# Kernel optimization log

Measured on AMD Instinct MI355X. Metric: run time of the kernel, lower is better.

The kernel has to match this reference:

```python
import jax, jax.numpy as jnp
import numpy as np

N, H, B, D, O = 512, 40, 8, 384, 62
DT = 1e-4  # step_size
BOUND = 500.0  # coupling saturation bound
# Jansen-Rit constants (ParamsJR defaults, all variances 0 -> non-learnable)
A_, a_, B_, b_, g_ = 3.25, 100.0, 22.0, 50.0, 100.0
c1, c2, c3, c4 = 135.0, 135.0 * 0.8, 135.0 * 0.25, 135.0 * 0.25
STD_IN, VMAX, V0, R_, MU, K_, KI = 100.0, 5.0, 6.0, 0.56, 0.5, 5.0, 1.0


def setup_inputs() -> dict:
    key = jax.random.key(0)
    ks = jax.random.split(key, 9)
    return {
        "input": jax.random.normal(ks[0], (N, H, B), jnp.float32),
        "noise_in": jax.random.normal(ks[1], (N, H, B, 1), jnp.float32),
        "noise_out": jax.random.normal(ks[2], (N, B), jnp.float32),
        "hx": jax.random.uniform(ks[3], (N, 6), jnp.float32),
        "hE": jax.random.normal(ks[4], (N, D), jnp.float32),
        "w_bb": jax.random.normal(ks[5], (N, N), jnp.float32),
        "sc": jax.random.uniform(ks[6], (N, N), jnp.float32),
        "lm": jax.random.normal(ks[7], (O, N), jnp.float32),
        "delays": jax.random.randint(ks[8], (N, N), 0, D, jnp.int32),
    }


def _sigmoid(x):
    # potential-to-rate operator
    return VMAX / (1.0 + jnp.exp(R_ * (V0 - x)))


def _sys2nd(Aamp, a, u, x, v):
    return Aamp * a * u - 2.0 * a * v - a * a * x


def reference(input, noise_in, noise_out, hx, hE, w_bb, sc, lm, delays):
    # normalized symmetric coupling matrix
    w = jnp.exp(w_bb) * sc
    ws = jnp.log1p(0.5 * (w + w.T))
    w_n = ws / jnp.linalg.norm(ws)            # Frobenius norm, as torch.linalg.norm
    rowsum = jnp.sum(w_n, axis=1)[:, None]    # dg = -diag(rowsum); dg @ x == -rowsum*x

    M, E, I = hx[:, 0:1], hx[:, 1:2], hx[:, 2:3]
    Mv, Ev, Iv = hx[:, 3:4], hx[:, 4:5], hx[:, 5:6]

    def hidden_step(carry, inp):
        M, E, I, Mv, Ev, Iv, hE = carry
        u, nz = inp  # [N,1] each
        Ed = jnp.take_along_axis(hE, delays, axis=1)      # Ed[i,j] = hE[i, delays[i,j]]
        LEd = jnp.sum(w_n * Ed.T, axis=1, keepdims=True)  # [N,1]
        noiseE = nz * STD_IN
        stim = K_ * KI * u
        rM = _sigmoid(E - I)
        rE = c2 * _sigmoid(c1 * M)
        rI = c4 * _sigmoid(c3 * M)
        coupled = g_ * (LEd - rowsum * (E - I))
        coupling = BOUND * jnp.tanh(coupled / BOUND)
        Mn = M + DT * Mv
        En = E + DT * Ev
        In = I + DT * Iv
        Mvn = Mv + DT * _sys2nd(A_, a_, rM, M, Mv)
        Evn = Ev + DT * _sys2nd(A_, a_, rE + coupling + stim + noiseE + MU, E, Ev)
        Ivn = Iv + DT * _sys2nd(B_, b_, rI, I, Iv)
        hE = hE.at[:, 0].set(En[:, 0] - In[:, 0])  # in-place slot-0 write, as in torch
        return (Mn, En, In, Mvn, Evn, Ivn, hE), None

    def batch_step(state, inp):
        u_seq, nz_seq = inp  # [H,N,1]
        state, _ = jax.lax.scan(hidden_step, state, (u_seq, nz_seq))
        M, E, I, Mv, Ev, Iv, hE = state
        hE = jnp.concatenate([E - I, hE[:, :-1]], axis=1)  # shift delay buffer
        eeg = 0.0005 * (lm @ (E - I))  # [O,1]
        return (M, E, I, Mv, Ev, Iv, hE), (M, E, I, Mv, Ev, Iv, eeg)

    u_all = jnp.transpose(input, (2, 1, 0))[..., None]            # [B,H,N,1]
    nz_all = jnp.transpose(noise_in[..., 0], (2, 1, 0))[..., None]
    state0 = (M, E, I, Mv, Ev, Iv, hE)
    state, outs = jax.lax.scan(batch_step, state0, (u_all, nz_all))
    Ms, Es, Is, Mvs, Evs, Ivs, eegs = outs  # [B,N,1] each, eeg [B,O,1]

    stack = lambda x: x[..., 0].T  # -> [N,B] (or [O,B]), matches torch.cat(axis=1)
    Mf, Ef, If, Mvf, Evf, Ivf, hEf = state
    current_state = jnp.concatenate([Mf, Ef, If, Mvf, Evf, Ivf], axis=1)  # [N,6]
    return (current_state, stack(eegs), stack(Es), stack(Is), stack(Ms),
            stack(Evs), stack(Ivs), stack(Mvs), hEf)
```

## Files before the change

kernel.cpp:

```cpp
#include <hip/hip_runtime.h>
#include <math.h>

#define N_    512
#define H_    40
#define B_N   8
#define D_    384
#define O_    62
#define RW    392
#define SMAX  13
#define CMAX  28
#define DRVS  336

#define OUT_STATE 0
#define OUT_EEG   3072
#define OUT_ES    3568
#define OUT_IS    7664
#define OUT_MS    11760
#define OUT_EVS   15856
#define OUT_IVS   19952
#define OUT_MVS   24048
#define OUT_HE    28144

#define SIGK      0.8079092228978195f
#define SIGC      4.847455337386917f
#define SIGK_E    109.06774509120563f
#define SIGK_I    27.266936272801407f
#define TANHS     0.5770780163555854f
#define C3Q       4.190944e-05f

#define BARRIER() asm volatile("s_waitcnt lgkmcnt(0)\n\ts_barrier" ::: "memory")

__global__ void k_cnt(const int* __restrict__ delays, int* __restrict__ s0c) {
    int i = blockIdx.x, t = threadIdx.x;
    bool f1 = (delays[t * N_ + i] == 0);
    bool f2 = (delays[(t + 256) * N_ + i] == 0);
    unsigned long long m1 = __ballot(f1), m2 = __ballot(f2);
    __shared__ int pc[4];
    int wave = t >> 6, lane = t & 63;
    if (lane == 0) pc[wave] = __popcll(m1) + __popcll(m2);
    __syncthreads();
    if (t == 0) {
        int s = pc[0] + pc[1] + pc[2] + pc[3];
        s0c[i] = (s > SMAX) ? SMAX : s;
    }
}

__global__ void __launch_bounds__(512)
k_perm(const int* __restrict__ s0c, int* __restrict__ perm,
       int* __restrict__ invp, int* __restrict__ wmaxc) {
    int t = threadIdx.x;
    int wave = t >> 6, lane = t & 63;
    int cnt = s0c[t];
    __shared__ int wc[14 * 8];
    __shared__ int base[14 * 8];
    unsigned long long below = (lane == 0) ? 0ull : ((~0ull) >> (64 - lane));
    for (int c = 0; c < 14; c++) {
        unsigned long long m = __ballot(cnt == c);
        if (lane == 0) wc[c * 8 + wave] = __popcll(m);
    }
    __syncthreads();
    if (t == 0) {
        int s = 0;
        for (int c = 0; c < 14; c++)
            for (int w = 0; w < 8; w++) { base[c * 8 + w] = s; s += wc[c * 8 + w]; }
    }
    __syncthreads();
    int pos = 0;
    for (int c = 0; c < 14; c++) {
        unsigned long long m = __ballot(cnt == c);
        if (cnt == c) pos = base[c * 8 + wave] + __popcll(m & below);
    }
    perm[pos] = t;
    invp[t] = pos;
    if ((pos & 63) == 63) wmaxc[pos >> 6] = cnt;
}

__global__ void k_prep(const float* __restrict__ wbb, const float* __restrict__ sc,
                       const float* __restrict__ hE_in, const int* __restrict__ delays,
                       const int* __restrict__ invp,
                       float* __restrict__ ws, float* __restrict__ ring,
                       float* __restrict__ rowsumP, float* __restrict__ sumsq,
                       float* __restrict__ s0w, int* __restrict__ s0j,
                       float* __restrict__ s1w, int* __restrict__ s1p) {
    int i = blockIdx.x;
    int t = threadIdx.x;
    int ip = invp[i];
    __shared__ float wsrow[N_];
    __shared__ float red[256];
    __shared__ int cnt_c[8];
    __shared__ int bases[8];
    __shared__ int runbase;

    if (t < SMAX) { s0j[t * N_ + ip] = i;        s0w[t * N_ + ip] = 0.f; }
    if (t < CMAX) { s1p[t * N_ + ip] = (1 << 9); s1w[t * N_ + ip] = 0.f; }
    if (t < 9)    { ring[i * RW + t] = 0.f; }

    float ssq = 0.f, rsum = 0.f;
    for (int j = t; j < N_; j += 256) {
        float w = 0.5f * (__expf(wbb[i * N_ + j]) * sc[i * N_ + j] +
                          __expf(wbb[j * N_ + i]) * sc[j * N_ + i]);
        float v = 0.6931471805599453f * __builtin_amdgcn_logf(1.0f + w);
        ws[i * N_ + j] = v;
        wsrow[j] = v;
        ssq += v * v;
        rsum += v;
    }
    for (int k = t; k < D_ - 1; k += 256) ring[i * RW + 9 + k] = hE_in[i * D_ + 1 + k];

    red[t] = ssq; __syncthreads();
    for (int s = 128; s > 0; s >>= 1) { if (t < s) red[t] += red[t + s]; __syncthreads(); }
    if (t == 0) sumsq[i] = red[0];
    __syncthreads();
    red[t] = rsum; __syncthreads();
    for (int s = 128; s > 0; s >>= 1) { if (t < s) red[t] += red[t + s]; __syncthreads(); }
    if (t == 0) rowsumP[ip] = red[0];
    __syncthreads();

    int wave = t >> 6, lane = t & 63;
    int dv1 = delays[t * N_ + i];
    int dv2 = delays[(t + 256) * N_ + i];
    unsigned long long below = (lane == 0) ? 0ull : ((~0ull) >> (64 - lane));
    for (int d = 0; d < 8; d++) {
        bool f1 = (dv1 == d), f2 = (dv2 == d);
        unsigned long long m1 = __ballot(f1);
        unsigned long long m2 = __ballot(f2);
        if (lane == 0) { cnt_c[wave] = __popcll(m1); cnt_c[wave + 4] = __popcll(m2); }
        __syncthreads();
        if (t == 0) {
            int s = (d == 0) ? 0 : runbase;
            for (int c = 0; c < 8; c++) { bases[c] = s; s += cnt_c[c]; }
            if (d == 0) runbase = 0;
            else runbase = s;
        }
        __syncthreads();
        if (d == 0) {
            if (f1) { int pos = bases[wave]     + __popcll(m1 & below);
                      if (pos < SMAX) { s0j[pos * N_ + ip] = t;       s0w[pos * N_ + ip] = wsrow[t]; } }
            if (f2) { int pos = bases[wave + 4] + __popcll(m2 & below);
                      if (pos < SMAX) { s0j[pos * N_ + ip] = t + 256; s0w[pos * N_ + ip] = wsrow[t + 256]; } }
        } else {
            if (f1) { int pos = bases[wave]     + __popcll(m1 & below);
                      if (pos < CMAX) { s1p[pos * N_ + ip] = t | (d << 9);         s1w[pos * N_ + ip] = wsrow[t]; } }
            if (f2) { int pos = bases[wave + 4] + __popcll(m2 & below);
                      if (pos < CMAX) { s1p[pos * N_ + ip] = (t + 256) | (d << 9); s1w[pos * N_ + ip] = wsrow[t + 256]; } }
        }
    }
}

__global__ void __launch_bounds__(512)
k_hist(const float* __restrict__ ws, const int* __restrict__ delays,
       const float* __restrict__ ring, const int* __restrict__ invp,
       const float* __restrict__ input, const float* __restrict__ noise_in,
       float* __restrict__ drv, float* __restrict__ bp8) {
    if (blockIdx.x < H_ * B_N) {
        int bb = blockIdx.x & 7, h = blockIdx.x >> 3;
        int step = bb * H_ + h;
        int nn = threadIdx.x;
        float u  = input[nn * (H_ * B_N) + h * B_N + bb];
        float nz = noise_in[nn * (H_ * B_N) + h * B_N + bb];
        drv[(size_t)invp[nn] * DRVS + step] = fmaf(0.1625f, u, fmaf(3.25f, nz, 16.26625f));
    }
    int b  = blockIdx.x >> 6;
    int ib = (blockIdx.x >> 3) & 7;
    int jb = blockIdx.x & 7;
    int wave = threadIdx.x >> 6, lane = threadIdx.x & 63;
    int i = ib * 64 + lane;
    int off = 8 - b;
    float acc = 0.f;
    int j0 = jb * 64 + wave * 8;
#pragma unroll
    for (int jj = 0; jj < 8; jj++) {
        int j = j0 + jj;
        int d = delays[j * N_ + i];
        float w = ws[j * N_ + i];
        float v = ring[j * RW + off + d];
        acc += (d > 0 ? w : 0.f) * v;
    }
    __shared__ float part[8][64];
    part[wave][lane] = acc; __syncthreads();
    if (wave == 0) {
        float s = 0.f;
#pragma unroll
        for (int w2 = 0; w2 < 8; w2++) s += part[w2][lane];
        bp8[(b * 8 + jb) * N_ + invp[i]] = s;
    }
}

#define LOADK0(K) int jb_##K = s0j[K * N_ + t] << 2; float w_##K = s0w[K * N_ + t] * scale;
#define GS(SLOT, K) (*(const float*)((const char*)curr4 + ((SLOT) << 11) + jb_##K))

#define PRFS(S, SLOT)                                                          \
    if (wmax > 0) { g##S##0 = GS(SLOT,0); g##S##1 = GS(SLOT,1); }              \
    if (wmax > 2) { g##S##2 = GS(SLOT,2); g##S##3 = GS(SLOT,3); }              \
    if (wmax > 4) { g##S##4 = GS(SLOT,4); g##S##5 = GS(SLOT,5);                \
                    g##S##6 = GS(SLOT,6); g##S##7 = GS(SLOT,7);                \
                    g##S##8 = GS(SLOT,8); g##S##9 = GS(SLOT,9);                \
                    g##S##10 = GS(SLOT,10); g##S##11 = GS(SLOT,11);            \
                    g##S##12 = GS(SLOT,12); }

#define STEPCORE(DV, S, WSLOT)                                                 \
  {                                                                            \
    float e0 = __builtin_amdgcn_exp2f(fmaf(-SIGK, ei_c, SIGC));                \
    float uu = __builtin_amdgcn_exp2f(fmaf(-SIGK_I, M, SIGC));                 \
    float u2 = uu * uu;                                                        \
    float u4 = u2 * u2;                                                        \
    float rMr = __builtin_amdgcn_rcpf(1.0f + e0);                              \
    float rIr = __builtin_amdgcn_rcpf(1.0f + uu);                              \
    float rEr = __builtin_amdgcn_rcpf(fmaf(C3Q, u4, 1.0f));                    \
    float En = fmaf(1e-4f, Ev, E);                                             \
    float In = fmaf(1e-4f, Iv, I);                                             \
    float Mn = fmaf(1e-4f, Mv, M);                                             \
    float a0 = 0.f, a1 = 0.f;                                                  \
    if (wmax > 0) { a0 = w_0 * g##S##0; a1 = w_1 * g##S##1; }                  \
    if (wmax > 2) { a0 = fmaf(w_2, g##S##2, a0); a1 = fmaf(w_3, g##S##3, a1); }\
    if (wmax > 4) { a0 = fmaf(w_4,  g##S##4,  a0); a1 = fmaf(w_5,  g##S##5,  a1);\
                    a0 = fmaf(w_6,  g##S##6,  a0); a1 = fmaf(w_7,  g##S##7,  a1);\
                    a0 = fmaf(w_8,  g##S##8,  a0); a1 = fmaf(w_9,  g##S##9,  a1);\
                    a0 = fmaf(w_10, g##S##10, a0); a1 = fmaf(w_11, g##S##11, a1);\
                    a0 = fmaf(w_12, g##S##12, a0); }                           \
    float arg = fmaf(-rs, ei_c, base) + (a0 + a1);                             \
    float e1 = __builtin_amdgcn_exp2f(arg);                                    \
    float cr = __builtin_amdgcn_rcpf(1.0f + e1);                               \
    float Mvn = fmaf(0.1625f,  rMr, fmaf(0.98f, Mv, -M));                      \
    float Ivn = fmaf(18.5625f, rIr, fmaf(0.99f, Iv, -0.25f * I));              \
    float Evn = fmaf(-32.5f, cr, fmaf(17.55f, rEr, fmaf(0.98f, Ev, -E) + (DV)));\
    float En2 = fmaf(1e-4f, Evn, En);                                          \
    float In2 = fmaf(1e-4f, Ivn, In);                                          \
    curr4[WSLOT][n] = En2 - In2;                                               \
    M = Mn; E = En; I = In; Mv = Mvn; Ev = Evn; Iv = Ivn;                      \
    ei_c = En - In;                                                            \
  }

#define BLOCK(S0, S1, W0, W1, DVA, DVB)                                        \
    PRFS(A, S0)                                                                \
    PRFS(B, S1)                                                                \
    STEPCORE(DVA, A, W0)                                                       \
    STEPCORE(DVB, B, W1)                                                       \
    BARRIER();

__global__ void __launch_bounds__(512)
k_hidden(const float* __restrict__ drv, const float* __restrict__ hE_in,
         const float* __restrict__ hx, const float* __restrict__ bp8,
         const float* __restrict__ sumsq, const float* __restrict__ rowsumP,
         const float* __restrict__ s0w, const int* __restrict__ s0j,
         const float* __restrict__ s1w, const int* __restrict__ s1p,
         const int* __restrict__ perm, const int* __restrict__ wmaxc,
         float* __restrict__ ring, float* __restrict__ fing,
         float* __restrict__ out) {
    __shared__ float curr4[4][N_];
    __shared__ float fin_l[B_N * N_];
    __shared__ float red[N_];
    int t = threadIdx.x;
    int n = perm[t];
    int wmax = __builtin_amdgcn_readfirstlane(wmaxc[t >> 6]);

    red[t] = sumsq[t];
    __syncthreads();
    if (t < 64) {
        float s2 = 0.f;
#pragma unroll
        for (int q = 0; q < 8; q++) s2 += red[t + 64 * q];
#pragma unroll
        for (int off = 32; off > 0; off >>= 1) s2 += __shfl_xor(s2, off, 64);
        if (t == 0) red[0] = s2;
    }
    __syncthreads();
    float scale = TANHS / sqrtf(red[0]);

    LOADK0(0)  LOADK0(1)  LOADK0(2)  LOADK0(3)  LOADK0(4)  LOADK0(5)  LOADK0(6)
    LOADK0(7)  LOADK0(8)  LOADK0(9)  LOADK0(10) LOADK0(11) LOADK0(12)
    int   s1p_r[CMAX];
    float s1w_r[CMAX];
#pragma unroll
    for (int k = 0; k < CMAX; k++) { s1p_r[k] = s1p[k * N_ + t]; s1w_r[k] = s1w[k * N_ + t] * scale; }

    float M  = hx[n * 6 + 0], E  = hx[n * 6 + 1], I  = hx[n * 6 + 2];
    float Mv = hx[n * 6 + 3], Ev = hx[n * 6 + 4], Iv = hx[n * 6 + 5];
    float rs = rowsumP[t] * scale;

    float hp[8];
#pragma unroll
    for (int k = 0; k < 8; k++) hp[k] = bp8[k * N_ + t];

    float gA0=0.f,gA1=0.f,gA2=0.f,gA3=0.f,gA4=0.f,gA5=0.f,gA6=0.f,gA7=0.f,
          gA8=0.f,gA9=0.f,gA10=0.f,gA11=0.f,gA12=0.f;
    float gB0=0.f,gB1=0.f,gB2=0.f,gB3=0.f,gB4=0.f,gB5=0.f,gB6=0.f,gB7=0.f,
          gB8=0.f,gB9=0.f,gB10=0.f,gB11=0.f,gB12=0.f;

    float ei_c = E - I;
#pragma unroll
    for (int k = 0; k < B_N; k++) fin_l[k * N_ + t] = 0.f;
    curr4[0][n] = hE_in[n * D_];
    curr4[1][n] = fmaf(1e-4f, Ev, E) - fmaf(1e-4f, Iv, I);
    __syncthreads();

    for (int b = 0; b < B_N; b++) {
        float hist = (((hp[0] + hp[1]) + (hp[2] + hp[3])) +
                      ((hp[4] + hp[5]) + (hp[6] + hp[7]))) * scale;
        float corr = 0.f;
#pragma unroll
        for (int k = 0; k < CMAX; k++) {
            int p = s1p_r[k];
            int off = (((b + 8 - (p >> 9)) & 7) << 11) + ((p & 511) << 2);
            corr = fmaf(s1w_r[k], *(const float*)((const char*)fin_l + off), corr);
        }
        float base = hist + corr;

        int bn = (b < B_N - 1) ? b + 1 : b;
#pragma unroll
        for (int k = 0; k < 8; k++) hp[k] = bp8[(bn * 8 + k) * N_ + t];

        const float4* sp4 = (const float4*)(drv + (size_t)t * DRVS + b * H_);
        float4 dc = sp4[0];
        for (int q = 0; q < 10; q++) {
            float4 dn = sp4[q + 1];
            BLOCK(0, 1, 2, 3, dc.x, dc.y)
            BLOCK(2, 3, 0, 1, dc.z, dc.w)
            dc = dn;
        }

        float eif = ei_c;
        fin_l[b * N_ + n] = eif;
        out[OUT_ES  + n * B_N + b] = E;
        out[OUT_IS  + n * B_N + b] = I;
        out[OUT_MS  + n * B_N + b] = M;
        out[OUT_EVS + n * B_N + b] = Ev;
        out[OUT_IVS + n * B_N + b] = Iv;
        out[OUT_MVS + n * B_N + b] = Mv;
        ring[n * RW + (7 - b)] = eif;
        ring[n * RW + (8 - b)] = eif;
        fing[b * N_ + n] = eif;
        BARRIER();
    }

    out[n * 6 + 0] = M;  out[n * 6 + 1] = E;  out[n * 6 + 2] = I;
    out[n * 6 + 3] = Mv; out[n * 6 + 4] = Ev; out[n * 6 + 5] = Iv;
}

__global__ void k_post(const float* __restrict__ ring, const float* __restrict__ fing,
                       const float* __restrict__ lm, float* __restrict__ out) {
    int bi = blockIdx.x;
    int lane = threadIdx.x;
    if (bi < N_) {
#pragma unroll
        for (int q = 0; q < 6; q++) {
            int k = lane + 64 * q;
            if (k < D_) out[OUT_HE + bi * D_ + k] = ring[bi * RW + k];
        }
    } else {
        int o = bi - N_;
        float lv[8];
#pragma unroll
        for (int q = 0; q < 8; q++) lv[q] = lm[o * N_ + 64 * q + lane];
        for (int b = 0; b < B_N; b++) {
            float p = 0.f;
#pragma unroll
            for (int q = 0; q < 8; q++) p = fmaf(lv[q], fing[b * N_ + 64 * q + lane], p);
#pragma unroll
            for (int off = 32; off > 0; off >>= 1) p += __shfl_down(p, off, 64);
            if (lane == 0) out[OUT_EEG + o * B_N + b] = 0.0005f * p;
        }
    }
}

extern "C" void kernel_launch(void* const* d_in, const int* in_sizes, int n_in,
                              void* d_out, int out_size, void* d_ws, size_t ws_size,
                              hipStream_t stream) {
    const float* input    = (const float*)d_in[0];
    const float* noise_in = (const float*)d_in[1];
    const float* hx       = (const float*)d_in[3];
    const float* hE       = (const float*)d_in[4];
    const float* wbb      = (const float*)d_in[5];
    const float* sc       = (const float*)d_in[6];
    const float* lm       = (const float*)d_in[7];
    const int*   delays   = (const int*)d_in[8];
    float* out = (float*)d_out;

    float* F    = (float*)d_ws;
    float* drv  = F;
    float* wsm  = drv + 172032;
    float* ring = wsm + 262144;
    float* bp8  = ring + 200704;
    float* rswP = bp8 + 32768;
    float* ssq  = rswP + 512;
    float* s0w  = ssq + 512;
    int*   s0j  = (int*)(s0w + N_ * SMAX);
    float* s1w  = (float*)(s0j + N_ * SMAX);
    int*   s1p  = (int*)(s1w + N_ * CMAX);
    float* fing = (float*)(s1p + N_ * CMAX);
    int*   s0c  = (int*)(fing + B_N * N_);
    int*   perm = s0c + N_;
    int*   invp = perm + N_;
    int*   wmaxc = invp + N_;

    k_cnt<<<N_, 256, 0, stream>>>(delays, s0c);
    k_perm<<<1, N_, 0, stream>>>(s0c, perm, invp, wmaxc);
    k_prep<<<N_, 256, 0, stream>>>(wbb, sc, hE, delays, invp,
                                   wsm, ring, rswP, ssq, s0w, s0j, s1w, s1p);
    k_hist<<<512, 512, 0, stream>>>(wsm, delays, ring, invp, input, noise_in, drv, bp8);
    k_hidden<<<1, N_, 0, stream>>>(drv, hE, hx, bp8, ssq, rswP,
                                   s0w, s0j, s1w, s1p, perm, wmaxc, ring, fing, out);
    k_post<<<N_ + O_, 64, 0, stream>>>(ring, fing, lm, out);
}
```

Measured before the change: 141.4 us.

## Drop node permutation kernels and compute per-wave zero-delay count in-kernel

Removes the k_cnt and k_perm launches that sorted nodes by zero-delay neighbour count. The count is now produced inside k_prep, and k_hidden takes a wave-wide max with shuffles instead of reading precomputed per-wave maxima. The gather prefetch and FMA chain now always do the first 8 slots unconditionally and branch only above 8. This saves two kernel launches and the indirection through perm and invp, but without sorting, waves may hold mixed counts and end up doing more gather work per step in the serial hidden loop.

```diff
diff --git a/kernel.cpp b/kernel.cpp
--- a/kernel.cpp
+++ b/kernel.cpp
@@ -30,69 +30,22 @@
 
 #define BARRIER() asm volatile("s_waitcnt lgkmcnt(0)\n\ts_barrier" ::: "memory")
 
-__global__ void k_cnt(const int* __restrict__ delays, int* __restrict__ s0c) {
-    int i = blockIdx.x, t = threadIdx.x;
-    bool f1 = (delays[t * N_ + i] == 0);
-    bool f2 = (delays[(t + 256) * N_ + i] == 0);
-    unsigned long long m1 = __ballot(f1), m2 = __ballot(f2);
-    __shared__ int pc[4];
-    int wave = t >> 6, lane = t & 63;
-    if (lane == 0) pc[wave] = __popcll(m1) + __popcll(m2);
-    __syncthreads();
-    if (t == 0) {
-        int s = pc[0] + pc[1] + pc[2] + pc[3];
-        s0c[i] = (s > SMAX) ? SMAX : s;
-    }
-}
-
-__global__ void __launch_bounds__(512)
-k_perm(const int* __restrict__ s0c, int* __restrict__ perm,
-       int* __restrict__ invp, int* __restrict__ wmaxc) {
-    int t = threadIdx.x;
-    int wave = t >> 6, lane = t & 63;
-    int cnt = s0c[t];
-    __shared__ int wc[14 * 8];
-    __shared__ int base[14 * 8];
-    unsigned long long below = (lane == 0) ? 0ull : ((~0ull) >> (64 - lane));
-    for (int c = 0; c < 14; c++) {
-        unsigned long long m = __ballot(cnt == c);
-        if (lane == 0) wc[c * 8 + wave] = __popcll(m);
-    }
-    __syncthreads();
-    if (t == 0) {
-        int s = 0;
-        for (int c = 0; c < 14; c++)
-            for (int w = 0; w < 8; w++) { base[c * 8 + w] = s; s += wc[c * 8 + w]; }
-    }
-    __syncthreads();
-    int pos = 0;
-    for (int c = 0; c < 14; c++) {
-        unsigned long long m = __ballot(cnt == c);
-        if (cnt == c) pos = base[c * 8 + wave] + __popcll(m & below);
-    }
-    perm[pos] = t;
-    invp[t] = pos;
-    if ((pos & 63) == 63) wmaxc[pos >> 6] = cnt;
-}
-
 __global__ void k_prep(const float* __restrict__ wbb, const float* __restrict__ sc,
                        const float* __restrict__ hE_in, const int* __restrict__ delays,
-                       const int* __restrict__ invp,
                        float* __restrict__ ws, float* __restrict__ ring,
-                       float* __restrict__ rowsumP, float* __restrict__ sumsq,
-                       float* __restrict__ s0w, int* __restrict__ s0j,
+                       float* __restrict__ rowsum_ws, float* __restrict__ sumsq,
+                       float* __restrict__ s0w, int* __restrict__ s0j, int* __restrict__ s0c,
                        float* __restrict__ s1w, int* __restrict__ s1p) {
     int i = blockIdx.x;
     int t = threadIdx.x;
-    int ip = invp[i];
     __shared__ float wsrow[N_];
     __shared__ float red[256];
     __shared__ int cnt_c[8];
     __shared__ int bases[8];
     __shared__ int runbase;
 
-    if (t < SMAX) { s0j[t * N_ + ip] = i;        s0w[t * N_ + ip] = 0.f; }
-    if (t < CMAX) { s1p[t * N_ + ip] = (1 << 9); s1w[t * N_ + ip] = 0.f; }
+    if (t < SMAX) { s0j[t * N_ + i] = i;        s0w[t * N_ + i] = 0.f; }
+    if (t < CMAX) { s1p[t * N_ + i] = (1 << 9); s1w[t * N_ + i] = 0.f; }
     if (t < 9)    { ring[i * RW + t] = 0.f; }
 
     float ssq = 0.f, rsum = 0.f;
@@ -113,7 +66,7 @@
     __syncthreads();
     red[t] = rsum; __syncthreads();
     for (int s = 128; s > 0; s >>= 1) { if (t < s) red[t] += red[t + s]; __syncthreads(); }
-    if (t == 0) rowsumP[ip] = red[0];
+    if (t == 0) rowsum_ws[i] = red[0];
     __syncthreads();
 
     int wave = t >> 6, lane = t & 63;
@@ -129,27 +82,27 @@
         if (t == 0) {
             int s = (d == 0) ? 0 : runbase;
             for (int c = 0; c < 8; c++) { bases[c] = s; s += cnt_c[c]; }
-            if (d == 0) runbase = 0;
+            if (d == 0) { s0c[i] = (s > SMAX) ? SMAX : s; runbase = 0; }
             else runbase = s;
         }
         __syncthreads();
         if (d == 0) {
             if (f1) { int pos = bases[wave]     + __popcll(m1 & below);
-                      if (pos < SMAX) { s0j[pos * N_ + ip] = t;       s0w[pos * N_ + ip] = wsrow[t]; } }
+                      if (pos < SMAX) { s0j[pos * N_ + i] = t;       s0w[pos * N_ + i] = wsrow[t]; } }
             if (f2) { int pos = bases[wave + 4] + __popcll(m2 & below);
-                      if (pos < SMAX) { s0j[pos * N_ + ip] = t + 256; s0w[pos * N_ + ip] = wsrow[t + 256]; } }
+                      if (pos < SMAX) { s0j[pos * N_ + i] = t + 256; s0w[pos * N_ + i] = wsrow[t + 256]; } }
         } else {
             if (f1) { int pos = bases[wave]     + __popcll(m1 & below);
-                      if (pos < CMAX) { s1p[pos * N_ + ip] = t | (d << 9);         s1w[pos * N_ + ip] = wsrow[t]; } }
+                      if (pos < CMAX) { s1p[pos * N_ + i] = t | (d << 9);         s1w[pos * N_ + i] = wsrow[t]; } }
             if (f2) { int pos = bases[wave + 4] + __popcll(m2 & below);
-                      if (pos < CMAX) { s1p[pos * N_ + ip] = (t + 256) | (d << 9); s1w[pos * N_ + ip] = wsrow[t + 256]; } }
+                      if (pos < CMAX) { s1p[pos * N_ + i] = (t + 256) | (d << 9); s1w[pos * N_ + i] = wsrow[t + 256]; } }
         }
     }
 }
 
 __global__ void __launch_bounds__(512)
 k_hist(const float* __restrict__ ws, const int* __restrict__ delays,
-       const float* __restrict__ ring, const int* __restrict__ invp,
+       const float* __restrict__ ring,
        const float* __restrict__ input, const float* __restrict__ noise_in,
        float* __restrict__ drv, float* __restrict__ bp8) {
     if (blockIdx.x < H_ * B_N) {
@@ -158,7 +111,7 @@
         int nn = threadIdx.x;
         float u  = input[nn * (H_ * B_N) + h * B_N + bb];
         float nz = noise_in[nn * (H_ * B_N) + h * B_N + bb];
-        drv[(size_t)invp[nn] * DRVS + step] = fmaf(0.1625f, u, fmaf(3.25f, nz, 16.26625f));
+        drv[(size_t)nn * DRVS + step] = fmaf(0.1625f, u, fmaf(3.25f, nz, 16.26625f));
     }
     int b  = blockIdx.x >> 6;
     int ib = (blockIdx.x >> 3) & 7;
@@ -182,7 +135,7 @@
         float s = 0.f;
 #pragma unroll
         for (int w2 = 0; w2 < 8; w2++) s += part[w2][lane];
-        bp8[(b * 8 + jb) * N_ + invp[i]] = s;
+        bp8[(b * 8 + jb) * N_ + i] = s;
     }
 }
 
@@ -190,11 +143,10 @@
 #define GS(SLOT, K) (*(const float*)((const char*)curr4 + ((SLOT) << 11) + jb_##K))
 
 #define PRFS(S, SLOT)                                                          \
-    if (wmax > 0) { g##S##0 = GS(SLOT,0); g##S##1 = GS(SLOT,1); }              \
-    if (wmax > 2) { g##S##2 = GS(SLOT,2); g##S##3 = GS(SLOT,3); }              \
-    if (wmax > 4) { g##S##4 = GS(SLOT,4); g##S##5 = GS(SLOT,5);                \
-                    g##S##6 = GS(SLOT,6); g##S##7 = GS(SLOT,7);                \
-                    g##S##8 = GS(SLOT,8); g##S##9 = GS(SLOT,9);                \
+    g##S##0 = GS(SLOT,0); g##S##1 = GS(SLOT,1); g##S##2 = GS(SLOT,2);          \
+    g##S##3 = GS(SLOT,3); g##S##4 = GS(SLOT,4); g##S##5 = GS(SLOT,5);          \
+    g##S##6 = GS(SLOT,6); g##S##7 = GS(SLOT,7);                                \
+    if (wmax > 8) { g##S##8 = GS(SLOT,8); g##S##9 = GS(SLOT,9);                \
                     g##S##10 = GS(SLOT,10); g##S##11 = GS(SLOT,11);            \
                     g##S##12 = GS(SLOT,12); }
 
@@ -210,14 +162,15 @@
     float En = fmaf(1e-4f, Ev, E);                                             \
     float In = fmaf(1e-4f, Iv, I);                                             \
     float Mn = fmaf(1e-4f, Mv, M);                                             \
-    float a0 = 0.f, a1 = 0.f;                                                  \
-    if (wmax > 0) { a0 = w_0 * g##S##0; a1 = w_1 * g##S##1; }                  \
-    if (wmax > 2) { a0 = fmaf(w_2, g##S##2, a0); a1 = fmaf(w_3, g##S##3, a1); }\
-    if (wmax > 4) { a0 = fmaf(w_4,  g##S##4,  a0); a1 = fmaf(w_5,  g##S##5,  a1);\
-                    a0 = fmaf(w_6,  g##S##6,  a0); a1 = fmaf(w_7,  g##S##7,  a1);\
-                    a0 = fmaf(w_8,  g##S##8,  a0); a1 = fmaf(w_9,  g##S##9,  a1);\
-                    a0 = fmaf(w_10, g##S##10, a0); a1 = fmaf(w_11, g##S##11, a1);\
-                    a0 = fmaf(w_12, g##S##12, a0); }                           \
+    float a0 = fmaf(w_2, g##S##2, w_0 * g##S##0);                              \
+    float a1 = fmaf(w_3, g##S##3, w_1 * g##S##1);                              \
+    a0 = fmaf(w_4, g##S##4, a0); a1 = fmaf(w_5, g##S##5, a1);                  \
+    a0 = fmaf(w_6, g##S##6, a0); a1 = fmaf(w_7, g##S##7, a1);                  \
+    if (wmax > 8) {                                                            \
+        a0 = fmaf(w_8,  g##S##8,  a0); a1 = fmaf(w_9,  g##S##9,  a1);          \
+        a0 = fmaf(w_10, g##S##10, a0); a1 = fmaf(w_11, g##S##11, a1);          \
+        a0 = fmaf(w_12, g##S##12, a0);                                         \
+    }                                                                          \
     float arg = fmaf(-rs, ei_c, base) + (a0 + a1);                             \
     float e1 = __builtin_amdgcn_exp2f(arg);                                    \
     float cr = __builtin_amdgcn_rcpf(1.0f + e1);                               \
@@ -232,27 +185,35 @@
   }
 
 #define BLOCK(S0, S1, W0, W1, DVA, DVB)                                        \
+  {                                                                            \
     PRFS(A, S0)                                                                \
     PRFS(B, S1)                                                                \
     STEPCORE(DVA, A, W0)                                                       \
     STEPCORE(DVB, B, W1)                                                       \
-    BARRIER();
+    BARRIER();                                                                 \
+  }
 
 __global__ void __launch_bounds__(512)
 k_hidden(const float* __restrict__ drv, const float* __restrict__ hE_in,
          const float* __restrict__ hx, const float* __restrict__ bp8,
-         const float* __restrict__ sumsq, const float* __restrict__ rowsumP,
+         const float* __restrict__ sumsq, const float* __restrict__ rowsum_ws,
          const float* __restrict__ s0w, const int* __restrict__ s0j,
-         const float* __restrict__ s1w, const int* __restrict__ s1p,
-         const int* __restrict__ perm, const int* __restrict__ wmaxc,
-         float* __restrict__ ring, float* __restrict__ fing,
-         float* __restrict__ out) {
+         const int* __restrict__ s0c, const float* __restrict__ s1w,
+         const int* __restrict__ s1p, float* __restrict__ ring,
+         float* __restrict__ fing, float* __restrict__ out) {
     __shared__ float curr4[4][N_];
     __shared__ float fin_l[B_N * N_];
     __shared__ float red[N_];
     int t = threadIdx.x;
-    int n = perm[t];
-    int wmax = __builtin_amdgcn_readfirstlane(wmaxc[t >> 6]);
+    int n = t;
+
+    int m = s0c[t];
+#pragma unroll
+    for (int off = 32; off > 0; off >>= 1) {
+        int o = __shfl_xor(m, off, 64);
+        m = (o > m) ? o : m;
+    }
+    int wmax = __builtin_amdgcn_readfirstlane(m);
 
     red[t] = sumsq[t];
     __syncthreads();
@@ -276,7 +237,7 @@
 
     float M  = hx[n * 6 + 0], E  = hx[n * 6 + 1], I  = hx[n * 6 + 2];
     float Mv = hx[n * 6 + 3], Ev = hx[n * 6 + 4], Iv = hx[n * 6 + 5];
-    float rs = rowsumP[t] * scale;
+    float rs = rowsum_ws[t] * scale;
 
     float hp[8];
 #pragma unroll
@@ -381,24 +342,19 @@
     float* wsm  = drv + 172032;
     float* ring = wsm + 262144;
     float* bp8  = ring + 200704;
-    float* rswP = bp8 + 32768;
-    float* ssq  = rswP + 512;
+    float* rsw  = bp8 + 32768;
+    float* ssq  = rsw + 512;
     float* s0w  = ssq + 512;
     int*   s0j  = (int*)(s0w + N_ * SMAX);
     float* s1w  = (float*)(s0j + N_ * SMAX);
     int*   s1p  = (int*)(s1w + N_ * CMAX);
     float* fing = (float*)(s1p + N_ * CMAX);
     int*   s0c  = (int*)(fing + B_N * N_);
-    int*   perm = s0c + N_;
-    int*   invp = perm + N_;
-    int*   wmaxc = invp + N_;
-
-    k_cnt<<<N_, 256, 0, stream>>>(delays, s0c);
-    k_perm<<<1, N_, 0, stream>>>(s0c, perm, invp, wmaxc);
-    k_prep<<<N_, 256, 0, stream>>>(wbb, sc, hE, delays, invp,
-                                   wsm, ring, rswP, ssq, s0w, s0j, s1w, s1p);
-    k_hist<<<512, 512, 0, stream>>>(wsm, delays, ring, invp, input, noise_in, drv, bp8);
-    k_hidden<<<1, N_, 0, stream>>>(drv, hE, hx, bp8, ssq, rswP,
-                                   s0w, s0j, s1w, s1p, perm, wmaxc, ring, fing, out);
+
+    k_prep<<<N_, 256, 0, stream>>>(wbb, sc, hE, delays, wsm, ring, rsw, ssq,
+                                   s0w, s0j, s0c, s1w, s1p);
+    k_hist<<<512, 512, 0, stream>>>(wsm, delays, ring, input, noise_in, drv, bp8);
+    k_hidden<<<1, N_, 0, stream>>>(drv, hE, hx, bp8, ssq, rsw,
+                                   s0w, s0j, s0c, s1w, s1p, ring, fing, out);
     k_post<<<N_ + O_, 64, 0, stream>>>(ring, fing, lm, out);
 }
```

Result: slower. 145.1 us (+2.6%).
